# Performance work log

Measured on AMD Instinct MI355X. Metric: run time of the kernel, lower is better.

The kernel has to match this reference:

```python
import jax, jax.numpy as jnp
import numpy as np

B, T, N, D, F = 32, 12, 1024, 64, 16
KH, DH = 8, 8  # heads, per-head dim; D = KH*DH


def setup_inputs() -> dict:
    key = jax.random.key(0)
    ks = jax.random.split(key, 24)
    def w(i, fi, fo):
        return jax.random.normal(ks[i], (fi, fo), jnp.float32) * (fi ** -0.5)
    adj = jax.random.uniform(ks[0], (N, N), jnp.float32)
    adj = adj / jnp.sum(adj, axis=-1, keepdims=True)  # row-normalized dense adjacency
    z = lambda: jnp.zeros((D,), jnp.float32)
    return dict(
        X=jax.random.normal(ks[1], (B, T, N, D), jnp.float32),
        STE=jax.random.normal(ks[2], (B, T, N, D), jnp.float32),
        adj=adj,
        feat0=jax.random.normal(ks[3], (N, F), jnp.float32),
        feat1=jax.random.normal(ks[4], (N, F), jnp.float32),
        Wq0=w(5, F, D), Wk0=w(6, F, D), Wq1=w(7, F, D), Wk1=w(8, F, D),
        Wgcn=w(9, 4 * D, D), bgcn=z(),
        Wq=w(10, 2 * D, D), bq=z(), Wk=w(11, 2 * D, D), bk=z(), Wv=w(12, 2 * D, D), bv=z(),
        Wx1=w(13, D, D), bx1=z(), Wx2=w(14, D, D), bx2=z(),
        Ws=w(15, D, D), Wt=w(16, D, D), bt=z(),
        Wh1=w(17, D, D), bh1=z(), Wh2=w(18, D, D), bh2=z(),
    )


def reference(X, STE, adj, feat0, feat1, Wq0, Wk0, Wq1, Wk1, Wgcn, bgcn,
              Wq, bq, Wk, bk, Wv, bv, Wx1, bx1, Wx2, bx2,
              Ws, Wt, bt, Wh1, bh1, Wh2, bh2):
    Dm = KH * DH
    # ---- graph conv: static adjacency + feature-driven softmax adjacencies ----
    parts = [X, jnp.einsum('mn,btnd->btmd', adj, X)]
    for feat, Wqf, Wkf in ((feat0, Wq0, Wk0), (feat1, Wq1, Wk1)):
        FEQ = jax.nn.relu(feat @ Wqf)            # [N, D]
        FEK = jax.nn.relu(feat @ Wkf)            # [N, D]
        S = jax.nn.softmax(FEQ @ FEK.T / jnp.sqrt(jnp.float32(Dm)), axis=-1)  # [N, N]
        parts.append(jnp.einsum('mn,btnd->btmd', S, X))
    HS = jax.nn.relu(jnp.concatenate(parts, -1) @ Wgcn + bgcn)  # [B,T,N,D]
    # ---- temporal multi-head self-attention over T ----
    Xc = jnp.concatenate([X, STE], -1)           # [B,T,N,2D]
    b, t, n, _ = Xc.shape
    q = jax.nn.relu(Xc @ Wq + bq).reshape(b, t, n, KH, DH)
    k = jax.nn.relu(Xc @ Wk + bk).reshape(b, t, n, KH, DH)
    v = jax.nn.relu(Xc @ Wv + bv).reshape(b, t, n, KH, DH)
    att = jnp.einsum('btnkd,bsnkd->bknts', q, k) / jnp.sqrt(jnp.float32(DH))
    att = jax.nn.softmax(att, axis=-1)           # [B,K,N,T,T]
    o = jnp.einsum('bknts,bsnkd->btnkd', att, v).reshape(b, t, n, Dm)
    HT = jax.nn.relu(o @ Wx1 + bx1) @ Wx2 + bx2
    # ---- gated fusion ----
    zg = jax.nn.sigmoid(HS @ Ws + HT @ Wt + bt)
    H = zg * HS + (1.0 - zg) * HT
    H = jax.nn.relu(H @ Wh1 + bh1) @ Wh2 + bh2
    return X + H
```

## Files before the change

### kernel.cpp

```cpp
#include <hip/hip_runtime.h>
#include <hip/hip_bf16.h>
#include <hip/hip_fp8.h>
#include <stdint.h>

#define B_ 32
#define T_ 12
#define N_ 1024
#define D_ 64
#define F_ 16
#define KH_ 8
#define BT_ (B_*T_)
#define NROWS_ (BT_*N_)
#define K3_ 3072

typedef unsigned short u16;
typedef unsigned char u8;
struct __align__(8) u16x4 { u16 x, y, z, w; };
struct __align__(16) u16x8 { u16 v[8]; };
typedef __attribute__((ext_vector_type(8))) short short8v;
typedef __attribute__((ext_vector_type(4))) float f32x4;
typedef __attribute__((ext_vector_type(2))) long long2v;

__device__ __forceinline__ float b2f(u16 u) {
  union { float f; unsigned int i; } c; c.i = ((unsigned int)u) << 16; return c.f;
}
__device__ __forceinline__ u16 f2b(float f) {
  union { float f; unsigned int i; } c; c.f = f;
  unsigned int u = c.i;
  unsigned int r = ((u >> 16) & 1u) + 0x7FFFu;
  return (u16)((u + r) >> 16);
}
__device__ __forceinline__ u8 f2e4(float f) {
  __hip_fp8_e4m3 h(f);
  return (u8)h.__x;
}
__device__ __forceinline__ unsigned cvt_pk_bf16(float lo, float hi) {
  unsigned r;
  asm volatile("v_cvt_pk_bf16_f32 %0, %1, %2" : "=v"(r) : "v"(lo), "v"(hi));
  return r;
}
__device__ __forceinline__ int kperm(int c) {
  int g = (c >> 3) & 7, e = c & 7;
  return (c & ~63) | ((g & 3) << 4) | ((g >> 2) << 3) | e;
}

__device__ __forceinline__ void gload_lds16(const void* g, void* l) {
  __builtin_amdgcn_global_load_lds(
      (const __attribute__((address_space(1))) unsigned int*)g,
      (__attribute__((address_space(3))) unsigned int*)l, 16, 0, 0);
}

__global__ __launch_bounds__(256) void k_pre(
    const float* __restrict__ feat0, const float* __restrict__ feat1,
    const float* __restrict__ Wq0, const float* __restrict__ Wk0,
    const float* __restrict__ Wq1, const float* __restrict__ Wk1,
    const float* __restrict__ adj,
    const float* __restrict__ Wq, const float* __restrict__ Wk,
    const float* __restrict__ Wv,
    const float* __restrict__ Wx1, const float* __restrict__ Wx2,
    const float* __restrict__ Ws, const float* __restrict__ Wt,
    const float* __restrict__ Wh1, const float* __restrict__ Wh2,
    const float* __restrict__ Wgcn,
    float* __restrict__ fe, float* __restrict__ feKt, u8* __restrict__ Acat8,
    u16* __restrict__ Wqkvt, u16* __restrict__ W1t, u16* __restrict__ W2t,
    u16* __restrict__ Wstt, u16* __restrict__ Wh1t, u16* __restrict__ Wh2t,
    u16* __restrict__ Wgcnt)
{
  int bid = blockIdx.x;
  int t = threadIdx.x;
  if (bid < 1024) {
    int r = bid;
    int m = t >> 6, d = t & 63;
    const float* feat = (m < 2) ? feat0 : feat1;
    const float* W = (m == 0) ? Wq0 : (m == 1) ? Wk0 : (m == 2) ? Wq1 : Wk1;
    float acc = 0.f;
    #pragma unroll
    for (int ff = 0; ff < F_; ++ff) acc += feat[r*F_ + ff] * W[ff*D_ + d];
    float val = fmaxf(acc, 0.f);
    fe[((size_t)m*N_ + r)*D_ + d] = val;
    if (m & 1) {
      int g = m >> 1;
      feKt[((size_t)g*D_ + d)*N_ + r] = val;
    }
  } else if (bid < 2048) {
    int r = bid - 1024;
    for (int c = t; c < N_; c += 256)
      Acat8[(size_t)r*K3_ + kperm(c)] = f2e4(adj[(size_t)r*N_ + c] * 256.0f);
  } else {
    int g0 = (bid - 2048)*256 + t;
    const int stride = 64*256;
    for (int i = g0; i < 192*128; i += stride) {
      int nn = i >> 7, kk = i & 127;
      const float* W = (nn < 64) ? Wq : (nn < 128) ? Wk : Wv;
      Wqkvt[i] = f2b(W[kk*64 + (nn & 63)]);
    }
    for (int i = g0; i < 64*64; i += stride) {
      int nn = i >> 6, kk = i & 63;
      W1t[i] = f2b(Wx1[kk*64 + nn]);
      W2t[i] = f2b(Wx2[kk*64 + nn]);
      Wh1t[i] = f2b(Wh1[kk*64 + nn]);
      Wh2t[i] = f2b(Wh2[kk*64 + nn]);
    }
    for (int i = g0; i < 64*128; i += stride) {
      int nn = i >> 7, kk = i & 127;
      Wstt[i] = f2b((kk < 64) ? Ws[kk*64 + nn] : Wt[(kk-64)*64 + nn]);
    }
    for (int i = g0; i < 256*64; i += stride) {
      int cc = i >> 6, kk = i & 63;
      Wgcnt[i] = f2b(Wgcn[(size_t)((cc >> 6)*64 + kk)*64 + (cc & 63)]);
    }
  }
}

__global__ __launch_bounds__(256) void k_graph_softmax(const float* __restrict__ fe,
                                                       const float* __restrict__ feKt,
                                                       u8* __restrict__ Acat8) {
  int r = blockIdx.x, g = blockIdx.y;
  const float* FEQ = fe + (size_t)(g*2 + 0)*N_*D_;
  const float* Kt  = feKt + (size_t)g*D_*N_;
  __shared__ float q[D_];
  __shared__ float red[256];
  int tid = threadIdx.x;
  if (tid < D_) q[tid] = FEQ[(size_t)r*D_ + tid];
  __syncthreads();
  float lg[4] = {0.f, 0.f, 0.f, 0.f};
  for (int f = 0; f < D_; ++f) {
    float qf = q[f];
    const float* kt = Kt + (size_t)f*N_;
    #pragma unroll
    for (int j = 0; j < 4; ++j) lg[j] += qf * kt[tid + j*256];
  }
  float mx = -1e30f;
  #pragma unroll
  for (int j = 0; j < 4; ++j) { lg[j] *= 0.125f; mx = fmaxf(mx, lg[j]); }
  red[tid] = mx; __syncthreads();
  for (int s = 128; s > 0; s >>= 1) { if (tid < s) red[tid] = fmaxf(red[tid], red[tid+s]); __syncthreads(); }
  mx = red[0]; __syncthreads();
  float sum = 0.f;
  #pragma unroll
  for (int j = 0; j < 4; ++j) { lg[j] = __expf(lg[j]-mx); sum += lg[j]; }
  red[tid] = sum; __syncthreads();
  for (int s = 128; s > 0; s >>= 1) { if (tid < s) red[tid] += red[tid+s]; __syncthreads(); }
  float inv = 256.0f / red[0];
  #pragma unroll
  for (int j = 0; j < 4; ++j) {
    int c = tid + j*256;
    Acat8[(size_t)r*K3_ + (1+g)*N_ + kperm(c)] = f2e4(lg[j]*inv);
  }
}

__global__ __launch_bounds__(256) void k_xw_mfma(
    const float* __restrict__ X, const u16* __restrict__ Wgcnt,
    u16* __restrict__ G0, u8* __restrict__ Yt1, u8* __restrict__ Yt2, u8* __restrict__ Yt3)
{
  __shared__ __align__(16) u16 SM[24576];
  u16* Als = SM;
  u16* Bls = SM + 8192;
  u8*  T8  = (u8*)SM;
  u16* Gls = SM;
  int m0 = blockIdx.x * 128;
  int t = threadIdx.x;
  int w = t >> 6, l = t & 63;

  {
    int rsub = l >> 3, pch = l & 7;
    #pragma unroll
    for (int i = 0; i < 8; ++i) {
      int R0 = w*64 + i*8;
      int n = R0 + rsub;
      int q = pch ^ (n & 7);
      gload_lds16(Wgcnt + (size_t)n*64 + q*8, &Bls[R0*64]);
    }
  }
  #pragma unroll
  for (int i = 0; i < 4; ++i) {
    int flat = t + 256*i;
    int row = flat >> 3, c = flat & 7;
    const float* src = X + (size_t)(m0+row)*64 + c*8;
    float4 f0 = *(const float4*)src;
    float4 f1 = *(const float4*)(src + 4);
    u16x8 pk;
    pk.v[0]=f2b(f0.x); pk.v[1]=f2b(f0.y); pk.v[2]=f2b(f0.z); pk.v[3]=f2b(f0.w);
    pk.v[4]=f2b(f1.x); pk.v[5]=f2b(f1.y); pk.v[6]=f2b(f1.z); pk.v[7]=f2b(f1.w);
    int cs = c ^ (row & 7);
    *(u16x8*)&Als[row*64 + cs*8] = pk;
  }
  __syncthreads();

  int wm = w & 1, wn = w >> 1;
  int lr = l & 15, lk = l >> 4;
  f32x4 acc[4][8] = {};
  #pragma unroll
  for (int ks = 0; ks < 2; ++ks) {
    short8v av[4], bv[8];
    #pragma unroll
    for (int fm = 0; fm < 4; ++fm) {
      int r = wm*64 + fm*16 + lr;
      int ch = (ks*4 + lk) ^ (r & 7);
      av[fm] = *(const short8v*)&Als[r*64 + ch*8];
    }
    #pragma unroll
    for (int fn = 0; fn < 8; ++fn) {
      int n = wn*128 + fn*16 + lr;
      int ch = (ks*4 + lk) ^ (n & 7);
      bv[fn] = *(const short8v*)&Bls[n*64 + ch*8];
    }
    #pragma unroll
    for (int fm = 0; fm < 4; ++fm)
      #pragma unroll
      for (int fn = 0; fn < 8; ++fn)
        acc[fm][fn] = __builtin_amdgcn_mfma_f32_16x16x32_bf16(av[fm], bv[fn], acc[fm][fn], 0, 0, 0);
  }
  __syncthreads();

  #pragma unroll
  for (int fm = 0; fm < 4; ++fm) {
    int row0 = wm*64 + fm*16 + lk*4;
    #pragma unroll
    for (int fn = 0; fn < 8; ++fn) {
      int c = wn*128 + fn*16 + lr;
      if (c >= 64) {
        int dp = c - 64;
        unsigned pk = (unsigned)f2e4(acc[fm][fn][0])
                    | ((unsigned)f2e4(acc[fm][fn][1]) << 8)
                    | ((unsigned)f2e4(acc[fm][fn][2]) << 16)
                    | ((unsigned)f2e4(acc[fm][fn][3]) << 24);
        *(unsigned*)&T8[dp*128 + (row0 ^ ((dp & 7) << 3))] = pk;
      }
    }
  }
  __syncthreads();
  {
    int bt = m0 >> 10, nb = m0 & 1023;
    #pragma unroll
    for (int i = 0; i < 12; ++i) {
      int cc = t + 256*i;
      int dp = cc >> 4, nc = cc & 15;
      int n0 = nc*8;
      unsigned long long v8 = *(const unsigned long long*)&T8[dp*128 + (n0 ^ ((dp & 7) << 3))];
      int p = dp >> 6, d = dp & 63;
      u8* Yt = (p == 0) ? Yt1 : (p == 1) ? Yt2 : Yt3;
      int gq = (n0 >> 3) & 7;
      int n0p = (n0 & ~63) | ((gq & 3) << 4) | ((gq >> 2) << 3);
      *(unsigned long long*)&Yt[((size_t)bt*64 + d)*1024 + nb + n0p] = v8;
    }
  }
  __syncthreads();

  if (wn == 0) {
    #pragma unroll
    for (int fm = 0; fm < 4; ++fm) {
      int row0 = wm*64 + fm*16 + lk*4;
      #pragma unroll
      for (int fn = 0; fn < 4; ++fn) {
        int c = fn*16 + lr;
        #pragma unroll
        for (int j = 0; j < 4; ++j) {
          int row = row0 + j;
          Gls[row*64 + (c ^ ((row & 7) << 3))] = f2b(acc[fm][fn][j]);
        }
      }
    }
  }
  __syncthreads();
  #pragma unroll
  for (int i = 0; i < 4; ++i) {
    int cc = t + 256*i;
    int row = cc >> 3, ch = cc & 7;
    u16x8 vv = *(const u16x8*)&Gls[row*64 + ((ch*8) ^ ((row & 7) << 3))];
    *(u16x8*)&G0[(size_t)(m0 + row)*64 + ch*8] = vv;
  }
}

#define BM 128
#define BK3 64
#define NKT3 (K3_/BK3)
__global__ __launch_bounds__(256) void k_spatial_mfma(
    const u8* __restrict__ Acat8,
    const u8* __restrict__ Yt1, const u8* __restrict__ Yt2, const u8* __restrict__ Yt3,
    const float* __restrict__ bgcn,
    u16* __restrict__ HS)
{
  __shared__ __align__(16) u8 SM8[32768];
  int f = blockIdx.x + 8*blockIdx.y;
  int u = f & 7, v = f >> 3;
  int btp = u*24 + (v >> 3);
  int m0  = (v & 7) * BM;
  int bt0 = btp * 2;

  int t = threadIdx.x;
  int w = t >> 6, l = t & 63;
  int rsub = l >> 2, pch = l & 3;

  f32x4 acc[4][4] = {};
  int wm = w >> 1, wn = w & 1;
  int lr = l & 15, lk = l >> 4;

  const u8* aSrc[2];
  size_t bOff[2];
  int R0s[2];
  #pragma unroll
  for (int i = 0; i < 2; ++i) {
    int row = w*32 + i*16 + rsub;
    int q = pch ^ ((row >> 1) & 3);
    aSrc[i] = Acat8 + (size_t)(m0 + row)*K3_ + q*16;
    int bt = bt0 + (row >> 6), d = row & 63;
    bOff[i] = ((size_t)bt*64 + d)*1024 + q*16;
    R0s[i] = w*32 + i*16;
  }

  #pragma unroll
  for (int i = 0; i < 2; ++i) {
    gload_lds16(aSrc[i], &SM8[R0s[i]*64]);
    gload_lds16(Yt1 + bOff[i], &SM8[16384 + R0s[i]*64]);
  }
  __syncthreads();

  int buf = 0;
  for (int kt = 0; kt < NKT3; ++kt) {
    if (kt + 1 < NKT3) {
      int k0 = (kt + 1) * BK3;
      int pl = k0 >> 10, kk = k0 & 1023;
      const u8* Yt = (pl == 0) ? Yt1 : (pl == 1) ? Yt2 : Yt3;
      int bo = (buf ^ 1) * 8192;
      #pragma unroll
      for (int i = 0; i < 2; ++i) {
        gload_lds16(aSrc[i] + k0, &SM8[bo + R0s[i]*64]);
        gload_lds16(Yt + bOff[i] + kk, &SM8[16384 + bo + R0s[i]*64]);
      }
    }
    const u8* A8 = SM8 + buf*8192;
    const u8* B8 = SM8 + 16384 + buf*8192;
    long2v av[4], bv[4];
    #pragma unroll
    for (int fm = 0; fm < 4; ++fm) {
      int r = wm*64 + fm*16 + lr;
      int sl = lk ^ ((r >> 1) & 3);
      av[fm] = *(const long2v*)(A8 + r*64 + sl*16);
    }
    #pragma unroll
    for (int fn = 0; fn < 4; ++fn) {
      int n = wn*64 + fn*16 + lr;
      int sl = lk ^ ((n >> 1) & 3);
      bv[fn] = *(const long2v*)(B8 + n*64 + sl*16);
    }
    #pragma unroll
    for (int ks = 0; ks < 2; ++ks)
      #pragma unroll
      for (int fm = 0; fm < 4; ++fm)
        #pragma unroll
        for (int fn = 0; fn < 4; ++fn)
          acc[fm][fn] = __builtin_amdgcn_mfma_f32_16x16x32_fp8_fp8(av[fm][ks], bv[fn][ks], acc[fm][fn], 0, 0, 0);
    __syncthreads();
    buf ^= 1;
  }

  u16* Tls = (u16*)SM8;
  #pragma unroll
  for (int fm = 0; fm < 4; ++fm) {
    #pragma unroll
    for (int fn = 0; fn < 4; ++fn) {
      int col = wn*64 + fn*16 + lr;
      int cc = col >> 3, cw = col & 7;
      #pragma unroll
      for (int j = 0; j < 4; ++j) {
        int node = wm*64 + fm*16 + lk*4 + j;
        int sc = cc ^ (node & 7);
        Tls[node*128 + sc*8 + cw] = f2b(acc[fm][fn][j] * 0.00390625f);
      }
    }
  }
  __syncthreads();
  #pragma unroll
  for (int i = 0; i < 8; ++i) {
    int flat = t + 256*i;
    int node = flat >> 4, cc = flat & 15;
    int sc = cc ^ (node & 7);
    u16x8 zv = *(const u16x8*)&Tls[node*128 + sc*8];
    int bt = bt0 + (cc >> 3), d0 = (cc & 7)*8;
    size_t idx = ((size_t)bt*N_ + (m0 + node))*64 + d0;
    u16x8 gv = *(const u16x8*)&HS[idx];
    float4 b0 = *(const float4*)&bgcn[d0];
    float4 b1 = *(const float4*)&bgcn[d0 + 4];
    float bb[8] = { b0.x, b0.y, b0.z, b0.w, b1.x, b1.y, b1.z, b1.w };
    u16x8 ov;
    #pragma unroll
    for (int e = 0; e < 8; ++e) {
      float vv2 = b2f(zv.v[e]) + b2f(gv.v[e]) + bb[e];
      ov.v[e] = f2b(fmaxf(vv2, 0.f));
    }
    *(u16x8*)&HS[idx] = ov;
  }
}

__global__ __launch_bounds__(256) void k_qkv(
    const float* __restrict__ X, const float* __restrict__ STE,
    const u16* __restrict__ Wqkvt,
    const float* __restrict__ bq, const float* __restrict__ bk, const float* __restrict__ bv,
    u16* __restrict__ qb, u16* __restrict__ kb, u16* __restrict__ vb)
{
  __shared__ __align__(16) u16 Als[128*128];
  __shared__ __align__(16) u16 Bls[192*128];
  int m0 = blockIdx.x * 128;
  int t = threadIdx.x;
  int w = t >> 6, l = t & 63;

  {
    int rsub = l >> 4, pch = l & 15;
    #pragma unroll
    for (int i = 0; i < 12; ++i) {
      int R0 = w*48 + i*4;
      int n = R0 + rsub;
      int sq = pch ^ (n & 7);
      gload_lds16(Wqkvt + (size_t)n*128 + sq*8, &Bls[R0*128]);
    }
  }
  #pragma unroll
  for (int i = 0; i < 8; ++i) {
    int flat = t + 256*i;
    int row = flat >> 4, c = flat & 15;
    const float* src = ((c < 8) ? X : STE) + (size_t)(m0+row)*64 + (c & 7)*8;
    float4 f0 = *(const float4*)src;
    float4 f1 = *(const float4*)(src + 4);
    u16x8 pk;
    pk.v[0]=f2b(f0.x); pk.v[1]=f2b(f0.y); pk.v[2]=f2b(f0.z); pk.v[3]=f2b(f0.w);
    pk.v[4]=f2b(f1.x); pk.v[5]=f2b(f1.y); pk.v[6]=f2b(f1.z); pk.v[7]=f2b(f1.w);
    int cs = c ^ (row & 7);
    *(u16x8*)&Als[row*128 + cs*8] = pk;
  }
  __syncthreads();

  int wm = w >> 1, wn = w & 1;
  int lr = l & 15, lk = l >> 4;
  f32x4 acc[4][6] = {};
  #pragma unroll
  for (int ks = 0; ks < 4; ++ks) {
    short8v av[4], bvv[6];
    #pragma unroll
    for (int fm = 0; fm < 4; ++fm) {
      int r = wm*64 + fm*16 + lr;
      int ch = (ks*4 + lk) ^ (r & 7);
      av[fm] = *(const short8v*)&Als[r*128 + ch*8];
    }
    #pragma unroll
    for (int fn = 0; fn < 6; ++fn) {
      int n = wn*96 + fn*16 + lr;
      int ch = (ks*4 + lk) ^ (n & 7);
      bvv[fn] = *(const short8v*)&Bls[n*128 + ch*8];
    }
    #pragma unroll
    for (int fm = 0; fm < 4; ++fm)
      #pragma unroll
      for (int fn = 0; fn < 6; ++fn)
        acc[fm][fn] = __builtin_amdgcn_mfma_f32_16x16x32_bf16(av[fm], bvv[fn], acc[fm][fn], 0, 0, 0);
  }

  #pragma unroll
  for (int fm = 0; fm < 4; ++fm) {
    int rowb = m0 + wm*64 + fm*16 + lk*4;
    #pragma unroll
    for (int fn = 0; fn < 6; ++fn) {
      int col = wn*96 + fn*16 + lr;
      int sel = col >> 6, d = col & 63;
      u16* dst = (sel == 0) ? qb : (sel == 1) ? kb : vb;
      float bias = ((sel == 0) ? bq : (sel == 1) ? bk : bv)[d];
      #pragma unroll
      for (int j = 0; j < 4; ++j) {
        float val = acc[fm][fn][j] + bias;
        dst[(size_t)(rowb + j)*64 + d] = f2b(fmaxf(val, 0.f));
      }
    }
  }
}

__global__ __launch_bounds__(256) void k_attn_ht(
    const u16* __restrict__ qb, const u16* __restrict__ kb, const u16* __restrict__ vb,
    const u16* __restrict__ W1t, const u16* __restrict__ W2t,
    const float* __restrict__ bx1, const float* __restrict__ bx2,
    u16* __restrict__ HT)
{
  __shared__ __align__(16) u16 QS[4][12*64];
  __shared__ __align__(16) u16 KS[4][12*64];
  __shared__ __align__(16) u16 VT[4][64*24];
  __shared__ __align__(16) u16 Ols[48*64];
  __shared__ __align__(16) u16 H1ls[48*64];
  __shared__ __align__(16) u16 W1ls[64*64];
  __shared__ __align__(16) u16 W2ls[64*64];
  int t = threadIdx.x;
  int w = t >> 6, l = t & 63;

  {
    int rsub = l >> 3, pch = l & 7;
    #pragma unroll
    for (int i = 0; i < 2; ++i) {
      int R0 = w*16 + i*8;
      int row = R0 + rsub;
      int sq = pch ^ (row & 7);
      gload_lds16(W1t + (size_t)row*64 + sq*8, &W1ls[R0*64]);
      gload_lds16(W2t + (size_t)row*64 + sq*8, &W2ls[R0*64]);
    }
  }

  int flat = blockIdx.x*4 + w;
  int b = flat >> 10, n = flat & 1023;
  {
    int ch = l >> 3, e = l & 7;
    #pragma unroll
    for (int tt = 0; tt < T_; ++tt) {
      size_t idx = ((size_t)(b*T_ + tt)*N_ + n)*64 + l;
      u16 qv = qb[idx], kv = kb[idx], vv = vb[idx];
      int sl = (ch ^ (tt & 7))*8 + e;
      QS[w][tt*64 + sl] = qv;
      KS[w][tt*64 + sl] = kv;
      VT[w][l*24 + tt] = vv;
    }
    #pragma unroll
    for (int tt = T_; tt < 16; ++tt) VT[w][l*24 + tt] = 0;
  }
  __syncthreads();

  int g = l >> 4;
  int sr = l & 15;
  short8v z8 = {0,0,0,0,0,0,0,0};
  float scale = 0.3535533906f;

  for (int h = 0; h < KH_; ++h) {
    short8v kf = *(const short8v*)&KS[w][sr*64 + ((h ^ (sr & 7)) << 3)];
    short8v qf = *(const short8v*)&QS[w][sr*64 + ((h ^ (sr & 7)) << 3)];
    short8v avk = (l < 16) ? kf : z8;
    short8v bvq = (l < 16) ? qf : z8;
    f32x4 zc = {0.f, 0.f, 0.f, 0.f};
    f32x4 S = __builtin_amdgcn_mfma_f32_16x16x32_bf16(avk, bvq, zc, 0, 0, 0);
    float sc0 = S[0]*scale, sc1 = S[1]*scale, sc2 = S[2]*scale, sc3 = S[3]*scale;
    bool gv = (g < 3);
    float mown = gv ? fmaxf(fmaxf(sc0, sc1), fmaxf(sc2, sc3)) : -1e30f;
    float m1 = fmaxf(mown, __shfl_xor(mown, 16));
    float m2 = fmaxf(m1, __shfl_xor(m1, 48));
    float e0 = gv ? __expf(sc0 - m2) : 0.f;
    float e1 = gv ? __expf(sc1 - m2) : 0.f;
    float e2 = gv ? __expf(sc2 - m2) : 0.f;
    float e3 = gv ? __expf(sc3 - m2) : 0.f;
    float ss = e0 + e1 + e2 + e3;
    float s1 = ss + __shfl_xor(ss, 16);
    float s2 = s1 + __shfl_xor(s1, 48);
    float rn = 1.0f / s2;
    float p0 = e0*rn, p1 = e1*rn, p2 = e2*rn, p3 = e3*rn;
    float pa0 = __shfl_xor(p0, 16), pa1 = __shfl_xor(p1, 16),
          pa2 = __shfl_xor(p2, 16), pa3 = __shfl_xor(p3, 16);
    float pb0 = __shfl_xor(p0, 48), pb1 = __shfl_xor(p1, 48),
          pb2 = __shfl_xor(p2, 48), pb3 = __shfl_xor(p3, 48);
    float v0, v1, v2, v3, v4, v5, v6, v7;
    if (g == 0)      { v0=p0;  v1=p1;  v2=p2;  v3=p3;  v4=pa0; v5=pa1; v6=pa2; v7=pa3; }
    else if (g == 1) { v0=pb0; v1=pb1; v2=pb2; v3=pb3; v4=0;   v5=0;   v6=0;   v7=0;   }
    else             { v0=0; v1=0; v2=0; v3=0; v4=0; v5=0; v6=0; v7=0; }
    union { unsigned u[4]; short8v s; } pk;
    pk.u[0] = cvt_pk_bf16(v0, v1);
    pk.u[1] = cvt_pk_bf16(v2, v3);
    pk.u[2] = cvt_pk_bf16(v4, v5);
    pk.u[3] = cvt_pk_bf16(v6, v7);
    int vrow = h*8 + (l & 7);
    short8v vf = *(const short8v*)&VT[w][vrow*24 + ((l >> 4) & 1)*8];
    short8v av2 = (g < 2) ? vf : z8;
    f32x4 O = __builtin_amdgcn_mfma_f32_16x16x32_bf16(av2, pk.s, zc, 0, 0, 0);
    if (g < 2 && sr < T_) {
      int r = w*T_ + sr;
      unsigned lo = cvt_pk_bf16(O[0], O[1]);
      unsigned hi = cvt_pk_bf16(O[2], O[3]);
      unsigned off = (unsigned)(r*64 + ((h ^ (r & 7)) << 3) + g*4);
      uint2 pr; pr.x = lo; pr.y = hi;
      *(uint2*)&Ols[off] = pr;
    }
  }
  __syncthreads();

  int lr = l & 15, lk = l >> 4;
  int col = w*16 + lr;
  f32x4 acc1[3] = {};
  #pragma unroll
  for (int ks = 0; ks < 2; ++ks) {
    short8v av[3], bvv;
    #pragma unroll
    for (int fm = 0; fm < 3; ++fm) {
      int r = fm*16 + lr;
      int ch = (ks*4 + lk) ^ (r & 7);
      av[fm] = *(const short8v*)&Ols[r*64 + ch*8];
    }
    {
      int nn = w*16 + lr;
      int ch = (ks*4 + lk) ^ (nn & 7);
      bvv = *(const short8v*)&W1ls[nn*64 + ch*8];
    }
    #pragma unroll
    for (int fm = 0; fm < 3; ++fm)
      acc1[fm] = __builtin_amdgcn_mfma_f32_16x16x32_bf16(av[fm], bvv, acc1[fm], 0, 0, 0);
  }
  {
    float bias1 = bx1[col];
    #pragma unroll
    for (int fm = 0; fm < 3; ++fm)
      #pragma unroll
      for (int j = 0; j < 4; ++j) {
        int r = fm*16 + lk*4 + j;
        H1ls[r*64 + ((col >> 3) ^ (r & 7))*8 + (col & 7)] = f2b(fmaxf(acc1[fm][j] + bias1, 0.f));
      }
  }
  __syncthreads();

  f32x4 acc2[3] = {};
  #pragma unroll
  for (int ks = 0; ks < 2; ++ks) {
    short8v av[3], bvv;
    #pragma unroll
    for (int fm = 0; fm < 3; ++fm) {
      int r = fm*16 + lr;
      int ch = (ks*4 + lk) ^ (r & 7);
      av[fm] = *(const short8v*)&H1ls[r*64 + ch*8];
    }
    {
      int nn = w*16 + lr;
      int ch = (ks*4 + lk) ^ (nn & 7);
      bvv = *(const short8v*)&W2ls[nn*64 + ch*8];
    }
    #pragma unroll
    for (int fm = 0; fm < 3; ++fm)
      acc2[fm] = __builtin_amdgcn_mfma_f32_16x16x32_bf16(av[fm], bvv, acc2[fm], 0, 0, 0);
  }
  {
    float bias2 = bx2[col];
    #pragma unroll
    for (int fm = 0; fm < 3; ++fm)
      #pragma unroll
      for (int j = 0; j < 4; ++j) {
        int r = fm*16 + lk*4 + j;
        int fp = blockIdx.x*4 + (r / T_);
        int tt = r % T_;
        int b2 = fp >> 10, n2 = fp & 1023;
        HT[((size_t)(b2*T_ + tt)*N_ + n2)*64 + col] = f2b(acc2[fm][j] + bias2);
      }
  }
}

__global__ __launch_bounds__(256) void k_fusion_mfma(
    const float* __restrict__ X,
    const u16* __restrict__ HS, const u16* __restrict__ HT,
    const u16* __restrict__ Wstt, const u16* __restrict__ Wh1t, const u16* __restrict__ Wh2t,
    const float* __restrict__ btb, const float* __restrict__ bh1, const float* __restrict__ bh2,
    float* __restrict__ out)
{
  __shared__ __align__(16) u16 Als[128*128];
  __shared__ __align__(16) u16 Wst[64*128];
  __shared__ __align__(16) u16 W1ls[64*64];
  __shared__ __align__(16) u16 W2ls[64*64];
  __shared__ __align__(16) u16 Hls[128*64];
  int m0 = blockIdx.x * 128;
  int t = threadIdx.x;
  int w = t >> 6, l = t & 63;

  {
    int rsub = l >> 4, pch = l & 15;
    #pragma unroll
    for (int i = 0; i < 8; ++i) {
      int R0 = w*32 + i*4;
      int row = R0 + rsub;
      int q = pch ^ (row & 7);
      const u16* src = (q < 8) ? (HS + (size_t)(m0 + row)*64 + q*8)
                               : (HT + (size_t)(m0 + row)*64 + (q - 8)*8);
      gload_lds16(src, &Als[R0*128]);
    }
    #pragma unroll
    for (int i = 0; i < 4; ++i) {
      int R0 = w*16 + i*4;
      int n = R0 + rsub;
      int q = pch ^ (n & 7);
      gload_lds16(Wstt + (size_t)n*128 + q*8, &Wst[R0*128]);
    }
  }
  {
    int rsub = l >> 3, pch = l & 7;
    #pragma unroll
    for (int i = 0; i < 2; ++i) {
      int R0 = w*16 + i*8;
      int row = R0 + rsub;
      int q = pch ^ (row & 7);
      gload_lds16(Wh1t + (size_t)row*64 + q*8, &W1ls[R0*64]);
      gload_lds16(Wh2t + (size_t)row*64 + q*8, &W2ls[R0*64]);
    }
  }
  __syncthreads();

  int lr = l & 15, lk = l >> 4;
  f32x4 acc1[2][4] = {};
  #pragma unroll
  for (int ks = 0; ks < 4; ++ks) {
    short8v av[2], bvv[4];
    #pragma unroll
    for (int fm = 0; fm < 2; ++fm) {
      int r = w*32 + fm*16 + lr;
      int ch = (ks*4 + lk) ^ (r & 7);
      av[fm] = *(const short8v*)&Als[r*128 + ch*8];
    }
    #pragma unroll
    for (int fn = 0; fn < 4; ++fn) {
      int n = fn*16 + lr;
      int ch = (ks*4 + lk) ^ (n & 7);
      bvv[fn] = *(const short8v*)&Wst[n*128 + ch*8];
    }
    #pragma unroll
    for (int fm = 0; fm < 2; ++fm)
      #pragma unroll
      for (int fn = 0; fn < 4; ++fn)
        acc1[fm][fn] = __builtin_amdgcn_mfma_f32_16x16x32_bf16(av[fm], bvv[fn], acc1[fm][fn], 0, 0, 0);
  }
  #pragma unroll
  for (int fm = 0; fm < 2; ++fm) {
    #pragma unroll
    for (int fn = 0; fn < 4; ++fn) {
      int col = fn*16 + lr;
      float bb = btb[col];
      #pragma unroll
      for (int j = 0; j < 4; ++j) {
        int row = w*32 + fm*16 + lk*4 + j;
        float a_s = acc1[fm][fn][j] + bb;
        float zg = 1.f/(1.f + __expf(-a_s));
        int cs = (col >> 3) ^ (row & 7);
        float hs = b2f(Als[row*128 + cs*8 + (col & 7)]);
        float ht = b2f(Als[row*128 + (cs + 8)*8 + (col & 7)]);
        float H = zg*hs + (1.f - zg)*ht;
        Hls[row*64 + cs*8 + (col & 7)] = f2b(H);
      }
    }
  }
  __syncthreads();

  u16* H2ls = Wst;
  f32x4 acc2[2][4] = {};
  #pragma unroll
  for (int ks = 0; ks < 2; ++ks) {
    short8v av[2], bvv[4];
    #pragma unroll
    for (int fm = 0; fm < 2; ++fm) {
      int r = w*32 + fm*16 + lr;
      int ch = (ks*4 + lk) ^ (r & 7);
      av[fm] = *(const short8v*)&Hls[r*64 + ch*8];
    }
    #pragma unroll
    for (int fn = 0; fn < 4; ++fn) {
      int n = fn*16 + lr;
      int ch = (ks*4 + lk) ^ (n & 7);
      bvv[fn] = *(const short8v*)&W1ls[n*64 + ch*8];
    }
    #pragma unroll
    for (int fm = 0; fm < 2; ++fm)
      #pragma unroll
      for (int fn = 0; fn < 4; ++fn)
        acc2[fm][fn] = __builtin_amdgcn_mfma_f32_16x16x32_bf16(av[fm], bvv[fn], acc2[fm][fn], 0, 0, 0);
  }
  __syncthreads();
  #pragma unroll
  for (int fm = 0; fm < 2; ++fm) {
    #pragma unroll
    for (int fn = 0; fn < 4; ++fn) {
      int col = fn*16 + lr;
      float bias = bh1[col];
      #pragma unroll
      for (int j = 0; j < 4; ++j) {
        int row = w*32 + fm*16 + lk*4 + j;
        float val = acc2[fm][fn][j] + bias;
        int cs = (col >> 3) ^ (row & 7);
        H2ls[row*64 + cs*8 + (col & 7)] = f2b(fmaxf(val, 0.f));
      }
    }
  }
  __syncthreads();

  f32x4 acc3[2][4] = {};
  #pragma unroll
  for (int ks = 0; ks < 2; ++ks) {
    short8v av[2], bvv[4];
    #pragma unroll
    for (int fm = 0; fm < 2; ++fm) {
      int r = w*32 + fm*16 + lr;
      int ch = (ks*4 + lk) ^ (r & 7);
      av[fm] = *(const short8v*)&H2ls[r*64 + ch*8];
    }
    #pragma unroll
    for (int fn = 0; fn < 4; ++fn) {
      int n = fn*16 + lr;
      int ch = (ks*4 + lk) ^ (n & 7);
      bvv[fn] = *(const short8v*)&W2ls[n*64 + ch*8];
    }
    #pragma unroll
    for (int fm = 0; fm < 2; ++fm)
      #pragma unroll
      for (int fn = 0; fn < 4; ++fn)
        acc3[fm][fn] = __builtin_amdgcn_mfma_f32_16x16x32_bf16(av[fm], bvv[fn], acc3[fm][fn], 0, 0, 0);
  }
  #pragma unroll
  for (int fm = 0; fm < 2; ++fm) {
    #pragma unroll
    for (int fn = 0; fn < 4; ++fn) {
      int col = fn*16 + lr;
      float bias = bh2[col];
      #pragma unroll
      for (int j = 0; j < 4; ++j) {
        int row = w*32 + fm*16 + lk*4 + j;
        size_t gi = (size_t)(m0 + row)*64 + col;
        out[gi] = X[gi] + acc3[fm][fn][j] + bias;
      }
    }
  }
}

extern "C" void kernel_launch(void* const* d_in, const int* in_sizes, int n_in,
                              void* d_out, int out_size, void* d_ws, size_t ws_size,
                              hipStream_t stream) {
  const float* X    = (const float*)d_in[0];
  const float* STE  = (const float*)d_in[1];
  const float* adj  = (const float*)d_in[2];
  const float* feat0= (const float*)d_in[3];
  const float* feat1= (const float*)d_in[4];
  const float* Wq0  = (const float*)d_in[5];
  const float* Wk0  = (const float*)d_in[6];
  const float* Wq1  = (const float*)d_in[7];
  const float* Wk1  = (const float*)d_in[8];
  const float* Wgcn = (const float*)d_in[9];
  const float* bgcn = (const float*)d_in[10];
  const float* Wq   = (const float*)d_in[11];
  const float* bq   = (const float*)d_in[12];
  const float* Wk   = (const float*)d_in[13];
  const float* bk   = (const float*)d_in[14];
  const float* Wv   = (const float*)d_in[15];
  const float* bv   = (const float*)d_in[16];
  const float* Wx1  = (const float*)d_in[17];
  const float* bx1  = (const float*)d_in[18];
  const float* Wx2  = (const float*)d_in[19];
  const float* bx2  = (const float*)d_in[20];
  const float* Ws   = (const float*)d_in[21];
  const float* Wt   = (const float*)d_in[22];
  const float* btb  = (const float*)d_in[23];
  const float* Wh1  = (const float*)d_in[24];
  const float* bh1  = (const float*)d_in[25];
  const float* Wh2  = (const float*)d_in[26];
  const float* bh2  = (const float*)d_in[27];
  (void)in_sizes; (void)n_in; (void)out_size;

  const size_t NEEDED = 164626432ull;
  if (ws_size < NEEDED) return;

  char* w = (char*)d_ws;
  float* fe    = (float*)(w);
  u8*    Acat8 = (u8*)(w + 1048576);
  u16*   Wqkvt = (u16*)(w + 7340032);
  u16*   W1t   = (u16*)(w + 7389184);
  u16*   W2t   = (u16*)(w + 7397376);
  u16*   Wstt  = (u16*)(w + 7405568);
  u16*   Wh1t  = (u16*)(w + 7421952);
  u16*   Wh2t  = (u16*)(w + 7430144);
  u16*   Wgcnt = (u16*)(w + 7438336);
  float* feKt  = (float*)(w + 7471104);
  u8*    Yt2   = (u8*)(w + 13631488);
  u8*    Yt3   = (u8*)(w + 63963136);
  u16*   HSb   = (u16*)(w + 114294784);
  u8*    Yt1   = (u8*)d_out;
  u16*   qb    = (u16*)(w + 13631488);
  u16*   kbuf  = (u16*)(w + 63963136);
  u16*   vbuf  = (u16*)d_out;
  u16*   HTb   = qb;

  k_pre<<<2112, 256, 0, stream>>>(feat0, feat1, Wq0, Wk0, Wq1, Wk1, adj,
                                  Wq, Wk, Wv, Wx1, Wx2, Ws, Wt, Wh1, Wh2, Wgcn,
                                  fe, feKt, Acat8, Wqkvt, W1t, W2t, Wstt, Wh1t, Wh2t, Wgcnt);
  k_graph_softmax<<<dim3(N_, 2), 256, 0, stream>>>(fe, feKt, Acat8);
  k_xw_mfma<<<NROWS_/128, 256, 0, stream>>>(X, Wgcnt, HSb, Yt1, Yt2, Yt3);
  k_spatial_mfma<<<dim3(8, BT_/2), 256, 0, stream>>>(Acat8, Yt1, Yt2, Yt3, bgcn, HSb);
  k_qkv<<<NROWS_/128, 256, 0, stream>>>(X, STE, Wqkvt, bq, bk, bv, qb, kbuf, vbuf);
  k_attn_ht<<<(B_*N_)/4, 256, 0, stream>>>(qb, kbuf, vbuf, W1t, W2t, bx1, bx2, HTb);
  k_fusion_mfma<<<NROWS_/128, 256, 0, stream>>>(X, HSb, HTb, Wstt, Wh1t, Wh2t,
                                                btb, bh1, bh2, (float*)d_out);
}
```

Before: 464.3 us.

## Fuse QKV projection into temporal attention kernel, drop q/k/v buffers

The separate k_qkv GEMM kernel is removed. Its work moves into k_attn_ht: each wave loads its node's 12 timesteps of X and STE, converts them to bf16 in LDS, and computes the Q/K/V projection with MFMA before writing straight into the per-wave QS/KS/VT tiles. This avoids writing and re-reading the large bf16 q/k/v intermediates through HBM and saves one kernel launch. In exchange, each wave reads the QKV weights directly from global memory (relying on cache), computes padded rows 12 to 15, and drops the block barrier because the staged data is only used within the same wave.

```diff
diff --git a/kernel.cpp b/kernel.cpp
--- a/kernel.cpp
+++ b/kernel.cpp
@@ -393,92 +393,15 @@
   }
 }
 
-__global__ __launch_bounds__(256) void k_qkv(
+__global__ __launch_bounds__(256) void k_attn_ht(
     const float* __restrict__ X, const float* __restrict__ STE,
     const u16* __restrict__ Wqkvt,
     const float* __restrict__ bq, const float* __restrict__ bk, const float* __restrict__ bv,
-    u16* __restrict__ qb, u16* __restrict__ kb, u16* __restrict__ vb)
-{
-  __shared__ __align__(16) u16 Als[128*128];
-  __shared__ __align__(16) u16 Bls[192*128];
-  int m0 = blockIdx.x * 128;
-  int t = threadIdx.x;
-  int w = t >> 6, l = t & 63;
-
-  {
-    int rsub = l >> 4, pch = l & 15;
-    #pragma unroll
-    for (int i = 0; i < 12; ++i) {
-      int R0 = w*48 + i*4;
-      int n = R0 + rsub;
-      int sq = pch ^ (n & 7);
-      gload_lds16(Wqkvt + (size_t)n*128 + sq*8, &Bls[R0*128]);
-    }
-  }
-  #pragma unroll
-  for (int i = 0; i < 8; ++i) {
-    int flat = t + 256*i;
-    int row = flat >> 4, c = flat & 15;
-    const float* src = ((c < 8) ? X : STE) + (size_t)(m0+row)*64 + (c & 7)*8;
-    float4 f0 = *(const float4*)src;
-    float4 f1 = *(const float4*)(src + 4);
-    u16x8 pk;
-    pk.v[0]=f2b(f0.x); pk.v[1]=f2b(f0.y); pk.v[2]=f2b(f0.z); pk.v[3]=f2b(f0.w);
-    pk.v[4]=f2b(f1.x); pk.v[5]=f2b(f1.y); pk.v[6]=f2b(f1.z); pk.v[7]=f2b(f1.w);
-    int cs = c ^ (row & 7);
-    *(u16x8*)&Als[row*128 + cs*8] = pk;
-  }
-  __syncthreads();
-
-  int wm = w >> 1, wn = w & 1;
-  int lr = l & 15, lk = l >> 4;
-  f32x4 acc[4][6] = {};
-  #pragma unroll
-  for (int ks = 0; ks < 4; ++ks) {
-    short8v av[4], bvv[6];
-    #pragma unroll
-    for (int fm = 0; fm < 4; ++fm) {
-      int r = wm*64 + fm*16 + lr;
-      int ch = (ks*4 + lk) ^ (r & 7);
-      av[fm] = *(const short8v*)&Als[r*128 + ch*8];
-    }
-    #pragma unroll
-    for (int fn = 0; fn < 6; ++fn) {
-      int n = wn*96 + fn*16 + lr;
-      int ch = (ks*4 + lk) ^ (n & 7);
-      bvv[fn] = *(const short8v*)&Bls[n*128 + ch*8];
-    }
-    #pragma unroll
-    for (int fm = 0; fm < 4; ++fm)
-      #pragma unroll
-      for (int fn = 0; fn < 6; ++fn)
-        acc[fm][fn] = __builtin_amdgcn_mfma_f32_16x16x32_bf16(av[fm], bvv[fn], acc[fm][fn], 0, 0, 0);
-  }
-
-  #pragma unroll
-  for (int fm = 0; fm < 4; ++fm) {
-    int rowb = m0 + wm*64 + fm*16 + lk*4;
-    #pragma unroll
-    for (int fn = 0; fn < 6; ++fn) {
-      int col = wn*96 + fn*16 + lr;
-      int sel = col >> 6, d = col & 63;
-      u16* dst = (sel == 0) ? qb : (sel == 1) ? kb : vb;
-      float bias = ((sel == 0) ? bq : (sel == 1) ? bk : bv)[d];
-      #pragma unroll
-      for (int j = 0; j < 4; ++j) {
-        float val = acc[fm][fn][j] + bias;
-        dst[(size_t)(rowb + j)*64 + d] = f2b(fmaxf(val, 0.f));
-      }
-    }
-  }
-}
-
-__global__ __launch_bounds__(256) void k_attn_ht(
-    const u16* __restrict__ qb, const u16* __restrict__ kb, const u16* __restrict__ vb,
     const u16* __restrict__ W1t, const u16* __restrict__ W2t,
     const float* __restrict__ bx1, const float* __restrict__ bx2,
     u16* __restrict__ HT)
 {
+  __shared__ __align__(16) u16 XC[4][16*128];
   __shared__ __align__(16) u16 QS[4][12*64];
   __shared__ __align__(16) u16 KS[4][12*64];
   __shared__ __align__(16) u16 VT[4][64*24];
@@ -503,21 +426,59 @@
 
   int flat = blockIdx.x*4 + w;
   int b = flat >> 10, n = flat & 1023;
+
   {
-    int ch = l >> 3, e = l & 7;
+    u16* xc = &XC[w][0];
+    int c0 = l, c1 = 64 + l;
     #pragma unroll
     for (int tt = 0; tt < T_; ++tt) {
-      size_t idx = ((size_t)(b*T_ + tt)*N_ + n)*64 + l;
-      u16 qv = qb[idx], kv = kb[idx], vv = vb[idx];
-      int sl = (ch ^ (tt & 7))*8 + e;
-      QS[w][tt*64 + sl] = qv;
-      KS[w][tt*64 + sl] = kv;
-      VT[w][l*24 + tt] = vv;
+      size_t rbase = ((size_t)(b*T_ + tt)*N_ + n)*64;
+      float xv = X[rbase + l];
+      float sv = STE[rbase + l];
+      xc[tt*128 + (((c0 >> 3) ^ (tt & 7)) << 3) + (c0 & 7)] = f2b(xv);
+      xc[tt*128 + (((c1 >> 3) ^ (tt & 7)) << 3) + (c1 & 7)] = f2b(sv);
+    }
+    #pragma unroll
+    for (int tt = T_; tt < 16; ++tt) {
+      xc[tt*128 + (((c0 >> 3) ^ (tt & 7)) << 3) + (c0 & 7)] = 0;
+      xc[tt*128 + (((c1 >> 3) ^ (tt & 7)) << 3) + (c1 & 7)] = 0;
+    }
+  }
+
+  int lr = l & 15, lk = l >> 4;
+
+  {
+    f32x4 accq[12];
+    #pragma unroll
+    for (int fn = 0; fn < 12; ++fn) accq[fn] = f32x4{0.f, 0.f, 0.f, 0.f};
+    #pragma unroll
+    for (int ks = 0; ks < 4; ++ks) {
+      short8v avx = *(const short8v*)&XC[w][lr*128 + (((ks*4 + lk) ^ (lr & 7)) << 3)];
+      #pragma unroll
+      for (int fn = 0; fn < 12; ++fn) {
+        short8v bvw = *(const short8v*)&Wqkvt[(size_t)(fn*16 + lr)*128 + (ks*4 + lk)*8];
+        accq[fn] = __builtin_amdgcn_mfma_f32_16x16x32_bf16(avx, bvw, accq[fn], 0, 0, 0);
+      }
+    }
+    #pragma unroll
+    for (int fn = 0; fn < 12; ++fn) {
+      int sel = fn >> 2;
+      int d = (fn & 3)*16 + lr;
+      float bias = ((sel == 0) ? bq : (sel == 1) ? bk : bv)[d];
+      #pragma unroll
+      for (int j = 0; j < 4; ++j) {
+        int tt = lk*4 + j;
+        if (tt < T_) {
+          u16 bv16 = f2b(fmaxf(accq[fn][j] + bias, 0.f));
+          if (sel == 0)      QS[w][tt*64 + (((d >> 3) ^ (tt & 7)) << 3) + (d & 7)] = bv16;
+          else if (sel == 1) KS[w][tt*64 + (((d >> 3) ^ (tt & 7)) << 3) + (d & 7)] = bv16;
+          else               VT[w][d*24 + tt] = bv16;
+        }
+      }
     }
     #pragma unroll
     for (int tt = T_; tt < 16; ++tt) VT[w][l*24 + tt] = 0;
   }
-  __syncthreads();
 
   int g = l >> 4;
   int sr = l & 15;
@@ -573,7 +534,6 @@
   }
   __syncthreads();
 
-  int lr = l & 15, lk = l >> 4;
   int col = w*16 + lr;
   f32x4 acc1[3] = {};
   #pragma unroll
@@ -862,10 +822,7 @@
   u8*    Yt3   = (u8*)(w + 63963136);
   u16*   HSb   = (u16*)(w + 114294784);
   u8*    Yt1   = (u8*)d_out;
-  u16*   qb    = (u16*)(w + 13631488);
-  u16*   kbuf  = (u16*)(w + 63963136);
-  u16*   vbuf  = (u16*)d_out;
-  u16*   HTb   = qb;
+  u16*   HTb   = (u16*)(w + 13631488);
 
   k_pre<<<2112, 256, 0, stream>>>(feat0, feat1, Wq0, Wk0, Wq1, Wk1, adj,
                                   Wq, Wk, Wv, Wx1, Wx2, Ws, Wt, Wh1, Wh2, Wgcn,
@@ -873,8 +830,8 @@
   k_graph_softmax<<<dim3(N_, 2), 256, 0, stream>>>(fe, feKt, Acat8);
   k_xw_mfma<<<NROWS_/128, 256, 0, stream>>>(X, Wgcnt, HSb, Yt1, Yt2, Yt3);
   k_spatial_mfma<<<dim3(8, BT_/2), 256, 0, stream>>>(Acat8, Yt1, Yt2, Yt3, bgcn, HSb);
-  k_qkv<<<NROWS_/128, 256, 0, stream>>>(X, STE, Wqkvt, bq, bk, bv, qb, kbuf, vbuf);
-  k_attn_ht<<<(B_*N_)/4, 256, 0, stream>>>(qb, kbuf, vbuf, W1t, W2t, bx1, bx2, HTb);
+  k_attn_ht<<<(B_*N_)/4, 256, 0, stream>>>(X, STE, Wqkvt, bq, bk, bv,
+                                           W1t, W2t, bx1, bx2, HTb);
   k_fusion_mfma<<<NROWS_/128, 256, 0, stream>>>(X, HSb, HTb, Wstt, Wh1t, Wh2t,
                                                 btb, bh1, bh2, (float*)d_out);
 }
```

New measurement: 595.9 us. 28.3% more time.
